# Optimization experiments

Measured on AMD Instinct MI355X. Metric: run time of the kernel, lower is better.

## Reference

```python
import jax, jax.numpy as jnp
from jax import lax
import numpy as np

N_NODES = 512
BATCH = 256
N_STEPS = 200
DT = 0.02  # t_span spacing; keeps 200 RK4 steps numerically tame


def setup_inputs() -> dict:
    key = jax.random.key(0)
    ks = jax.random.split(key, 7)
    s = 1.0 / np.sqrt(N_NODES)
    x_init = jax.random.normal(ks[0], (BATCH, N_NODES), dtype=jnp.float32)
    t_span = jnp.arange(N_STEPS, dtype=jnp.float32) * DT
    # MaskedLinear params (kaiming-uniform-ish scale)
    W1 = jax.random.uniform(ks[1], (N_NODES, N_NODES), jnp.float32, -s, s)
    b1 = jax.random.uniform(ks[2], (N_NODES,), jnp.float32, -s, s)
    # inner Linear params
    W2 = jax.random.uniform(ks[3], (N_NODES, N_NODES), jnp.float32, -s, s)
    b2 = jax.random.uniform(ks[4], (N_NODES,), jnp.float32, -s, s)
    mask = jax.random.bernoulli(ks[5], 0.1, (N_NODES, N_NODES)).astype(jnp.float32)
    mask = mask * (1.0 - jnp.eye(N_NODES, dtype=jnp.float32))
    return {"x_init": x_init, "t_span": t_span, "W1": W1, "b1": b1,
            "W2": W2, "b2": b2, "mask": mask}


def reference(x_init, t_span, W1, b1, W2, b2, mask):
    # ODE func: dydt = W2 @ tanh(masked(W1) @ y + b1) + b2 (t unused)
    Wm = W1 * mask  # [N, N]
    def f(y):  # y: [B, N]
        return jnp.tanh(y @ Wm.T + b1) @ W2.T + b2

    dts = t_span[1:] - t_span[:-1]  # [T-1]

    def rk4_step(y, dt):
        k1 = f(y)
        k2 = f(y + dt * k1 / 2)
        k3 = f(y + dt * k2 / 2)
        k4 = f(y + dt * k3)
        y_new = y + dt / 6 * (k1 + 2 * k2 + 2 * k3 + k4)
        return y_new, y_new

    _, traj = lax.scan(rk4_step, x_init, dts)  # [T-1, B, N]
    traj = jnp.concatenate([x_init[None], traj], axis=0)  # [T, B, N]
    return jnp.transpose(traj, (1, 0, 2))  # [B, T, N]
```

## Files before the change

### kernel.cpp

```cpp
#include <hip/hip_runtime.h>
#include <math.h>

#define NN 512
#define NB 256
#define NT 200
#define TPB 256
#define NTEAM 8

typedef unsigned long long u64;
typedef _Float16 half8 __attribute__((ext_vector_type(8)));
typedef float f32x4 __attribute__((ext_vector_type(4)));

#define WS_WM  0
#define WS_WC  (NN*NN)
#define WS_C   (WS_WC + NN*NN/2)
#define WS_X0  (WS_C + NN)
#define WS_HB0 (WS_X0 + NB*NN)
#define WS_CNT (WS_HB0 + NB*NN/2)

__device__ __forceinline__ void sysst_u64(u64* p, u64 v) {
  __hip_atomic_store(p, v, __ATOMIC_RELAXED, __HIP_MEMORY_SCOPE_SYSTEM);
}
__device__ __forceinline__ u64 sysld_u64(const u64* p) {
  return __hip_atomic_load(p, __ATOMIC_RELAXED, __HIP_MEMORY_SCOPE_SYSTEM);
}
__device__ __forceinline__ void sysst_f1(float* p, float v) {
  __hip_atomic_store(p, v, __ATOMIC_RELAXED, __HIP_MEMORY_SCOPE_SYSTEM);
}
__device__ __forceinline__ float sysld_f1(const float* p) {
  return __hip_atomic_load(p, __ATOMIC_RELAXED, __HIP_MEMORY_SCOPE_SYSTEM);
}
__device__ __forceinline__ void sysst_u16(unsigned short* p, unsigned short v) {
  __hip_atomic_store(p, v, __ATOMIC_RELAXED, __HIP_MEMORY_SCOPE_SYSTEM);
}
__device__ __forceinline__ void sysst_h(_Float16* p, float v) {
  union { _Float16 hf; unsigned short us; } cv; cv.hf = (_Float16)v;
  sysst_u16((unsigned short*)p, cv.us);
}

__global__ __launch_bounds__(256)
void k_init(const float* __restrict__ W1, const float* __restrict__ mask,
            const float* __restrict__ x_init, float* __restrict__ ws,
            float* __restrict__ out) {
  int gt = blockIdx.x * 256 + threadIdx.x;
  int stride = gridDim.x * 256;
  for (int i = gt; i < NN * NN; i += stride) ws[WS_WM + i] = W1[i] * mask[i];
  for (int i = gt; i < NB * NN / 2; i += stride) {
    u64 q = ((const u64*)x_init)[i];
    int r = i >> 8, np = i & 255;
    *((u64*)(out + (size_t)r * NT * NN) + np) = q;
  }
  if (gt < 64 * NTEAM * 16)
    __hip_atomic_store(((unsigned*)(ws + WS_CNT)) + gt, 0u,
                       __ATOMIC_RELAXED, __HIP_MEMORY_SCOPE_SYSTEM);
}

__global__ __launch_bounds__(128)
void k_prep(const float* __restrict__ W2g, const float* __restrict__ b2,
            const float* __restrict__ x_init, float* __restrict__ ws) {
  __shared__ float w1row[NN];
  const int j = blockIdx.x;
  const int t = threadIdx.x;
  const float* wm = ws + WS_WM + (size_t)j * NN;
  for (int i = t; i < NN; i += 128) w1row[i] = wm[i];
  __syncthreads();

  f32x4 acc = {0.f, 0.f, 0.f, 0.f};
  for (int m = 0; m < NN; ++m) {
    float w = w1row[m];
    if (w != 0.f)
      acc += w * ((const f32x4*)(W2g + (size_t)m * NN))[t];
  }
  _Float16* wcrow = (_Float16*)(ws + WS_WC) + (size_t)j * NN;
#pragma unroll
  for (int e = 0; e < 4; ++e) wcrow[4 * t + e] = (_Float16)acc[e];

  if (t == 0) {
    float s = 0.f;
    for (int m = 0; m < NN; ++m)
      if (w1row[m] != 0.f) s += b2[m] * w1row[m];
    ws[WS_C + j] = s;
  }

#pragma unroll
  for (int rr = 0; rr < 2; ++rr) {
    int r = t + rr * 128;
    const float* y0 = x_init + (size_t)r * NN;
    float s = 0.f;
    for (int m = 0; m < NN; ++m) {
      float w = w1row[m];
      if (w != 0.f) s = fmaf(y0[m], w, s);
    }
    sysst_f1(ws + WS_X0 + (size_t)r * NN + j, s);
  }
}

__device__ __forceinline__ void team_wait(unsigned* flagsp, unsigned target) {
  if (threadIdx.x < NTEAM) {
    while (__hip_atomic_load(flagsp + threadIdx.x * 16, __ATOMIC_RELAXED,
                             __HIP_MEMORY_SCOPE_AGENT) < target)
      __builtin_amdgcn_s_sleep(1);
  }
  __syncthreads();
}
__device__ __forceinline__ void team_release(unsigned* flagsp, int cg, unsigned e) {
  __syncthreads();
  if (threadIdx.x == 0)
    __hip_atomic_store(flagsp + cg * 16, e, __ATOMIC_RELAXED,
                       __HIP_MEMORY_SCOPE_SYSTEM);
}

struct St { u64 a0, a1; };
__device__ __forceinline__ St stage_load(const _Float16* __restrict__ src,
                                         int tid) {
  const int row = tid >> 6;
  const int g = tid & 63;
  const u64* s = (const u64*)(src + (size_t)row * NN) + g * 2;
  St v; v.a0 = sysld_u64(s); v.a1 = sysld_u64(s + 1);
  return v;
}
__device__ __forceinline__ void stage_write(_Float16* __restrict__ plane,
                                            const St& v, int tid) {
  const int row = tid >> 6;
  const int g = tid & 63;
  union { u64 q[2]; half8 h; } u; u.q[0] = v.a0; u.q[1] = v.a1;
  ((half8*)plane)[row * 64 + (g ^ row)] = u.h;
}

__device__ __forceinline__ void gemm8(const _Float16* plane, const _Float16* wb,
                                      int rc, int kg, int wv, float res[4]) {
  const int swzA = rc & 3;
  const int swzB = rc & 7;
  const half8* pA = (const half8*)plane;
  const half8* pB = (const half8*)wb;
  const int abase = (rc & 3) * 64;
  const int bbase = (wv * 16 + rc) * 64;
  f32x4 ae = {0.f, 0.f, 0.f, 0.f};
  f32x4 ao = {0.f, 0.f, 0.f, 0.f};
#pragma unroll
  for (int kt = 0; kt < 16; kt += 2) {
    const int k0 = kt * 4 + kg;
    const int k1 = (kt + 1) * 4 + kg;
    ae = __builtin_amdgcn_mfma_f32_16x16x32_f16(pA[abase + (k0 ^ swzA)],
                                                pB[bbase + (k0 ^ swzB)],
                                                ae, 0, 0, 0);
    ao = __builtin_amdgcn_mfma_f32_16x16x32_f16(pA[abase + (k1 ^ swzA)],
                                                pB[bbase + (k1 ^ swzB)],
                                                ao, 0, 0, 0);
  }
#pragma unroll
  for (int r = 0; r < 4; ++r) res[r] = ae[r] + ao[r];
}

__global__ __launch_bounds__(TPB, 1)
void k_ode(const float* __restrict__ tspan,
           const float* __restrict__ W2g,
           const float* __restrict__ b1,
           const float* __restrict__ b2,
           float* __restrict__ ws,
           float* __restrict__ out,
           const float* __restrict__ x_init) {
  extern __shared__ _Float16 ldsh[];
  _Float16* wc  = ldsh;
  _Float16* w2  = ldsh + 32768;
  _Float16* plA = ldsh + 65536;
  _Float16* plB = ldsh + 67584;

  const int bid = blockIdx.x;
  const int cg = bid & 7, rgA = bid >> 3;
  const int r0p[2] = {rgA * 4, rgA * 4 + 128};
  const int j0 = cg * 64;
  const int tid = threadIdx.x;
  const int lane = tid & 63, wv = tid >> 6;
  const int rc = lane & 15, kg = lane >> 4;
  const int mycol = j0 + wv * 16 + rc;
  const bool act = (kg == 0);

  unsigned* flbase = (unsigned*)(ws + WS_CNT);
  unsigned* flp[2] = {flbase + rgA * (NTEAM * 16),
                      flbase + (rgA + 32) * (NTEAM * 16)};
  _Float16* hb[2] = {(_Float16*)(ws + WS_HB0), (_Float16*)(ws + WS_WM)};

  {
    const int col = tid >> 2;
    const int part = tid & 3;
    const half8* s1 = (const half8*)((const _Float16*)(ws + WS_WC)
                                     + (size_t)(j0 + col) * NN) + part * 16;
    const float* s2 = W2g + (size_t)(j0 + col) * NN + part * 128;
    half8* d1 = (half8*)wc;
    half8* d2 = (half8*)w2;
    const int key = col & 7;
#pragma unroll
    for (int i = 0; i < 16; ++i) {
      int g = part * 16 + i;
      int idx = col * 64 + (g ^ key);
      d1[idx] = s1[i];
      half8 hv;
#pragma unroll
      for (int e = 0; e < 8; ++e) hv[e] = (_Float16)s2[i * 8 + e];
      d2[idx] = hv;
    }
  }
  const float b1s = b1[mycol], b2s = b2[mycol];
  const float c_own = ws[WS_C + mycol];

  float xb[2][4], yb[2][4], H[2][4];
  if (act) {
#pragma unroll
    for (int p = 0; p < 2; ++p)
#pragma unroll
      for (int r = 0; r < 4; ++r) {
        int row = r0p[p] + r;
        xb[p][r] = sysld_f1(ws + WS_X0 + (size_t)row * NN + mycol);
        yb[p][r] = x_init[(size_t)row * NN + mycol];
        float h = tanhf(xb[p][r] + b1s);
        H[p][r] = h;
        sysst_h(hb[0] + (size_t)row * NN + mycol, h);
      }
  }
  __syncthreads();
  if (tid == 0) {
    __hip_atomic_store(flp[0] + cg * 16, 1u, __ATOMIC_RELAXED,
                       __HIP_MEMORY_SCOPE_SYSTEM);
    __hip_atomic_store(flp[1] + cg * 16, 1u, __ATOMIC_RELAXED,
                       __HIP_MEMORY_SCOPE_SYSTEM);
  }

  float res[4], res2[4];

  for (int t = 0; t < NT - 1; ++t) {
    const float dt = tspan[t + 1] - tspan[t];
    const float c6 = dt / 6.0f;
#pragma unroll 1
    for (int s = 0; s < 4; ++s) {
      const int q = t * 4 + s;
      const unsigned target = (unsigned)(q + 1);
      const _Float16* rdb = hb[q & 1];
      _Float16* wrb = hb[(q + 1) & 1];

      team_wait(flp[0], target);
      St va = stage_load(rdb + (size_t)r0p[0] * NN, tid);
      team_wait(flp[1], target);
      St vb = stage_load(rdb + (size_t)r0p[1] * NN, tid);

      stage_write(plA, va, tid);
      __syncthreads();
      gemm8(plA, wc, rc, kg, wv, res);
      if (s == 3) gemm8(plA, w2, rc, kg, wv, res2);
      if (act) {
        if (s < 3) {
          const float a = (s == 2) ? dt : dt * 0.5f;
#pragma unroll
          for (int r = 0; r < 4; ++r) {
            float xs = xb[0][r] + a * (res[r] + c_own);
            float h = tanhf(xs + b1s);
            float st;
            if (s == 2) { H[0][r] += h;       st = H[0][r]; }
            else        { H[0][r] += 2.f * h; st = h;       }
            sysst_h(wrb + (size_t)(r0p[0] + r) * NN + mycol, st);
          }
        } else {
#pragma unroll
          for (int r = 0; r < 4; ++r) {
            int row = r0p[0] + r;
            xb[0][r] += c6 * res[r] + dt * c_own;
            yb[0][r] += c6 * res2[r] + dt * b2s;
            out[((size_t)row * NT + (t + 1)) * NN + mycol] = yb[0][r];
            float h = tanhf(xb[0][r] + b1s);
            H[0][r] = h;
            sysst_h(wrb + (size_t)row * NN + mycol, h);
          }
        }
      }
      team_release(flp[0], cg, target + 1);

      stage_write(plB, vb, tid);
      __syncthreads();
      gemm8(plB, wc, rc, kg, wv, res);
      if (s == 3) gemm8(plB, w2, rc, kg, wv, res2);
      if (act) {
        if (s < 3) {
          const float a = (s == 2) ? dt : dt * 0.5f;
#pragma unroll
          for (int r = 0; r < 4; ++r) {
            float xs = xb[1][r] + a * (res[r] + c_own);
            float h = tanhf(xs + b1s);
            float st;
            if (s == 2) { H[1][r] += h;       st = H[1][r]; }
            else        { H[1][r] += 2.f * h; st = h;       }
            sysst_h(wrb + (size_t)(r0p[1] + r) * NN + mycol, st);
          }
        } else {
#pragma unroll
          for (int r = 0; r < 4; ++r) {
            int row = r0p[1] + r;
            xb[1][r] += c6 * res[r] + dt * c_own;
            yb[1][r] += c6 * res2[r] + dt * b2s;
            out[((size_t)row * NT + (t + 1)) * NN + mycol] = yb[1][r];
            float h = tanhf(xb[1][r] + b1s);
            H[1][r] = h;
            sysst_h(wrb + (size_t)row * NN + mycol, h);
          }
        }
      }
      team_release(flp[1], cg, target + 1);
    }
  }
}

extern "C" void kernel_launch(void* const* d_in, const int* in_sizes, int n_in,
                              void* d_out, int out_size, void* d_ws, size_t ws_size,
                              hipStream_t stream) {
  const float* x_init = (const float*)d_in[0];
  const float* tspan  = (const float*)d_in[1];
  const float* W1     = (const float*)d_in[2];
  const float* b1     = (const float*)d_in[3];
  const float* W2     = (const float*)d_in[4];
  const float* b2     = (const float*)d_in[5];
  const float* mask   = (const float*)d_in[6];
  float* out = (float*)d_out;
  float* ws  = (float*)d_ws;

  hipLaunchKernelGGL(k_init, dim3(256), dim3(256), 0, stream,
                     W1, mask, x_init, ws, out);
  hipLaunchKernelGGL(k_prep, dim3(512), dim3(128), 0, stream,
                     W2, b2, x_init, ws);

  const unsigned ldsBytes = 136 * 1024;
  (void)hipFuncSetAttribute((const void*)k_ode,
                            hipFuncAttributeMaxDynamicSharedMemorySize,
                            (int)ldsBytes);

  hipLaunchKernelGGL(k_ode, dim3(256), dim3(TPB), ldsBytes, stream,
                     tspan, W2, b1, b2, ws, out, x_init);
}
```

Measured before the change: 2.668 ms.

## Replace team flag barriers with tagged data words for inter-block sync

Removes the per-team counter flags and the release/wait barriers. Each hidden-state exchange word now carries its step number in the upper 32 bits, next to two packed fp16 values, so consumers poll the data itself until every tag matches. The LDS staging planes are double-buffered by step parity so the release barrier can be dropped. This cuts flag round-trips and syncthreads per stage, at the cost of doubling exchange-buffer traffic (64-bit words for 2 halves) and extra shuffles to pack values.

```diff
diff --git a/kernel.cpp b/kernel.cpp
--- a/kernel.cpp
+++ b/kernel.cpp
@@ -5,7 +5,6 @@
 #define NB 256
 #define NT 200
 #define TPB 256
-#define NTEAM 8
 
 typedef unsigned long long u64;
 typedef _Float16 half8 __attribute__((ext_vector_type(8)));
@@ -16,7 +15,6 @@
 #define WS_C   (WS_WC + NN*NN/2)
 #define WS_X0  (WS_C + NN)
 #define WS_HB0 (WS_X0 + NB*NN)
-#define WS_CNT (WS_HB0 + NB*NN/2)
 
 __device__ __forceinline__ void sysst_u64(u64* p, u64 v) {
   __hip_atomic_store(p, v, __ATOMIC_RELAXED, __HIP_MEMORY_SCOPE_SYSTEM);
@@ -30,12 +28,10 @@
 __device__ __forceinline__ float sysld_f1(const float* p) {
   return __hip_atomic_load(p, __ATOMIC_RELAXED, __HIP_MEMORY_SCOPE_SYSTEM);
 }
-__device__ __forceinline__ void sysst_u16(unsigned short* p, unsigned short v) {
-  __hip_atomic_store(p, v, __ATOMIC_RELAXED, __HIP_MEMORY_SCOPE_SYSTEM);
-}
-__device__ __forceinline__ void sysst_h(_Float16* p, float v) {
-  union { _Float16 hf; unsigned short us; } cv; cv.hf = (_Float16)v;
-  sysst_u16((unsigned short*)p, cv.us);
+__device__ __forceinline__ u64 packh(float a, float b, unsigned tag) {
+  union { _Float16 h[2]; unsigned u; } lo;
+  lo.h[0] = (_Float16)a; lo.h[1] = (_Float16)b;
+  return ((u64)tag << 32) | (u64)lo.u;
 }
 
 __global__ __launch_bounds__(256)
@@ -50,9 +46,6 @@
     int r = i >> 8, np = i & 255;
     *((u64*)(out + (size_t)r * NT * NN) + np) = q;
   }
-  if (gt < 64 * NTEAM * 16)
-    __hip_atomic_store(((unsigned*)(ws + WS_CNT)) + gt, 0u,
-                       __ATOMIC_RELAXED, __HIP_MEMORY_SCOPE_SYSTEM);
 }
 
 __global__ __launch_bounds__(128)
@@ -95,36 +88,14 @@
   }
 }
 
-__device__ __forceinline__ void team_wait(unsigned* flagsp, unsigned target) {
-  if (threadIdx.x < NTEAM) {
-    while (__hip_atomic_load(flagsp + threadIdx.x * 16, __ATOMIC_RELAXED,
-                             __HIP_MEMORY_SCOPE_AGENT) < target)
-      __builtin_amdgcn_s_sleep(1);
-  }
-  __syncthreads();
-}
-__device__ __forceinline__ void team_release(unsigned* flagsp, int cg, unsigned e) {
-  __syncthreads();
-  if (threadIdx.x == 0)
-    __hip_atomic_store(flagsp + cg * 16, e, __ATOMIC_RELAXED,
-                       __HIP_MEMORY_SCOPE_SYSTEM);
-}
-
-struct St { u64 a0, a1; };
-__device__ __forceinline__ St stage_load(const _Float16* __restrict__ src,
-                                         int tid) {
-  const int row = tid >> 6;
-  const int g = tid & 63;
-  const u64* s = (const u64*)(src + (size_t)row * NN) + g * 2;
-  St v; v.a0 = sysld_u64(s); v.a1 = sysld_u64(s + 1);
-  return v;
-}
-__device__ __forceinline__ void stage_write(_Float16* __restrict__ plane,
-                                            const St& v, int tid) {
-  const int row = tid >> 6;
-  const int g = tid & 63;
-  union { u64 q[2]; half8 h; } u; u.q[0] = v.a0; u.q[1] = v.a1;
-  ((half8*)plane)[row * 64 + (g ^ row)] = u.h;
+__device__ __forceinline__ void unpack_write(_Float16* __restrict__ plane,
+                                             u64 v0, u64 v1, u64 v2, u64 v3,
+                                             int tid) {
+  const int row = tid >> 6, g = tid & 63;
+  union { unsigned u[4]; half8 h; } x;
+  x.u[0] = (unsigned)v0; x.u[1] = (unsigned)v1;
+  x.u[2] = (unsigned)v2; x.u[3] = (unsigned)v3;
+  ((half8*)plane)[row * 64 + (g ^ row)] = x.h;
 }
 
 __device__ __forceinline__ void gemm8(const _Float16* plane, const _Float16* wb,
@@ -161,10 +132,8 @@
            float* __restrict__ out,
            const float* __restrict__ x_init) {
   extern __shared__ _Float16 ldsh[];
-  _Float16* wc  = ldsh;
-  _Float16* w2  = ldsh + 32768;
-  _Float16* plA = ldsh + 65536;
-  _Float16* plB = ldsh + 67584;
+  _Float16* wc = ldsh;
+  _Float16* w2 = ldsh + 32768;
 
   const int bid = blockIdx.x;
   const int cg = bid & 7, rgA = bid >> 3;
@@ -176,10 +145,8 @@
   const int mycol = j0 + wv * 16 + rc;
   const bool act = (kg == 0);
 
-  unsigned* flbase = (unsigned*)(ws + WS_CNT);
-  unsigned* flp[2] = {flbase + rgA * (NTEAM * 16),
-                      flbase + (rgA + 32) * (NTEAM * 16)};
-  _Float16* hb[2] = {(_Float16*)(ws + WS_HB0), (_Float16*)(ws + WS_WM)};
+  u64* hbt0 = (u64*)(ws + WS_HB0);
+  u64* hbt1 = (u64*)(ws + WS_WM);
 
   {
     const int col = tid >> 2;
@@ -215,18 +182,16 @@
         yb[p][r] = x_init[(size_t)row * NN + mycol];
         float h = tanhf(xb[p][r] + b1s);
         H[p][r] = h;
-        sysst_h(hb[0] + (size_t)row * NN + mycol, h);
+        float hn = __shfl_down(h, 1);
+        if ((rc & 1) == 0)
+          sysst_u64(hbt0 + (size_t)row * 256 + (mycol >> 1), packh(h, hn, 0u));
       }
   }
   __syncthreads();
-  if (tid == 0) {
-    __hip_atomic_store(flp[0] + cg * 16, 1u, __ATOMIC_RELAXED,
-                       __HIP_MEMORY_SCOPE_SYSTEM);
-    __hip_atomic_store(flp[1] + cg * 16, 1u, __ATOMIC_RELAXED,
-                       __HIP_MEMORY_SCOPE_SYSTEM);
-  }
 
   float res[4], res2[4];
+  const int row_g = tid >> 6;
+  const int gidx = (tid & 63) * 4;
 
   for (int t = 0; t < NT - 1; ++t) {
     const float dt = tspan[t + 1] - tspan[t];
@@ -234,16 +199,29 @@
 #pragma unroll 1
     for (int s = 0; s < 4; ++s) {
       const int q = t * 4 + s;
-      const unsigned target = (unsigned)(q + 1);
-      const _Float16* rdb = hb[q & 1];
-      _Float16* wrb = hb[(q + 1) & 1];
-
-      team_wait(flp[0], target);
-      St va = stage_load(rdb + (size_t)r0p[0] * NN, tid);
-      team_wait(flp[1], target);
-      St vb = stage_load(rdb + (size_t)r0p[1] * NN, tid);
-
-      stage_write(plA, va, tid);
+      const unsigned wtag = (unsigned)(q + 1);
+      u64* rb = (q & 1) ? hbt1 : hbt0;
+      u64* wr = (q & 1) ? hbt0 : hbt1;
+      const u64* rdA = rb + (size_t)(r0p[0] + row_g) * 256 + gidx;
+      const u64* rdB = rb + (size_t)(r0p[1] + row_g) * 256 + gidx;
+      _Float16* plA = ldsh + 65536 + (q & 1) * 2048;
+      _Float16* plB = ldsh + 65536 + 4096 + (q & 1) * 2048;
+
+      u64 a0, a1, a2, a3;
+      for (;;) {
+        a0 = sysld_u64(rdA);     a1 = sysld_u64(rdA + 1);
+        a2 = sysld_u64(rdA + 2); a3 = sysld_u64(rdA + 3);
+        bool ok = ((unsigned)(a0 >> 32) == (unsigned)q) &
+                  ((unsigned)(a1 >> 32) == (unsigned)q) &
+                  ((unsigned)(a2 >> 32) == (unsigned)q) &
+                  ((unsigned)(a3 >> 32) == (unsigned)q);
+        if (__all(ok)) break;
+        __builtin_amdgcn_s_sleep(1);
+      }
+      u64 b0 = sysld_u64(rdB),       b1v_ = sysld_u64(rdB + 1);
+      u64 b2v_ = sysld_u64(rdB + 2), b3 = sysld_u64(rdB + 3);
+
+      unpack_write(plA, a0, a1, a2, a3, tid);
       __syncthreads();
       gemm8(plA, wc, rc, kg, wv, res);
       if (s == 3) gemm8(plA, w2, rc, kg, wv, res2);
@@ -257,7 +235,10 @@
             float st;
             if (s == 2) { H[0][r] += h;       st = H[0][r]; }
             else        { H[0][r] += 2.f * h; st = h;       }
-            sysst_h(wrb + (size_t)(r0p[0] + r) * NN + mycol, st);
+            float sn = __shfl_down(st, 1);
+            if ((rc & 1) == 0)
+              sysst_u64(wr + (size_t)(r0p[0] + r) * 256 + (mycol >> 1),
+                        packh(st, sn, wtag));
           }
         } else {
 #pragma unroll
@@ -268,13 +249,25 @@
             out[((size_t)row * NT + (t + 1)) * NN + mycol] = yb[0][r];
             float h = tanhf(xb[0][r] + b1s);
             H[0][r] = h;
-            sysst_h(wrb + (size_t)row * NN + mycol, h);
+            float hn = __shfl_down(h, 1);
+            if ((rc & 1) == 0)
+              sysst_u64(wr + (size_t)row * 256 + (mycol >> 1),
+                        packh(h, hn, wtag));
           }
         }
       }
-      team_release(flp[0], cg, target + 1);
-
-      stage_write(plB, vb, tid);
+
+      for (;;) {
+        bool ok = ((unsigned)(b0 >> 32) == (unsigned)q) &
+                  ((unsigned)(b1v_ >> 32) == (unsigned)q) &
+                  ((unsigned)(b2v_ >> 32) == (unsigned)q) &
+                  ((unsigned)(b3 >> 32) == (unsigned)q);
+        if (__all(ok)) break;
+        __builtin_amdgcn_s_sleep(1);
+        b0 = sysld_u64(rdB);       b1v_ = sysld_u64(rdB + 1);
+        b2v_ = sysld_u64(rdB + 2); b3 = sysld_u64(rdB + 3);
+      }
+      unpack_write(plB, b0, b1v_, b2v_, b3, tid);
       __syncthreads();
       gemm8(plB, wc, rc, kg, wv, res);
       if (s == 3) gemm8(plB, w2, rc, kg, wv, res2);
@@ -288,7 +281,10 @@
             float st;
             if (s == 2) { H[1][r] += h;       st = H[1][r]; }
             else        { H[1][r] += 2.f * h; st = h;       }
-            sysst_h(wrb + (size_t)(r0p[1] + r) * NN + mycol, st);
+            float sn = __shfl_down(st, 1);
+            if ((rc & 1) == 0)
+              sysst_u64(wr + (size_t)(r0p[1] + r) * 256 + (mycol >> 1),
+                        packh(st, sn, wtag));
           }
         } else {
 #pragma unroll
@@ -299,11 +295,13 @@
             out[((size_t)row * NT + (t + 1)) * NN + mycol] = yb[1][r];
             float h = tanhf(xb[1][r] + b1s);
             H[1][r] = h;
-            sysst_h(wrb + (size_t)row * NN + mycol, h);
+            float hn = __shfl_down(h, 1);
+            if ((rc & 1) == 0)
+              sysst_u64(wr + (size_t)row * 256 + (mycol >> 1),
+                        packh(h, hn, wtag));
           }
         }
       }
-      team_release(flp[1], cg, target + 1);
     }
   }
 }
@@ -326,7 +324,7 @@
   hipLaunchKernelGGL(k_prep, dim3(512), dim3(128), 0, stream,
                      W2, b2, x_init, ws);
 
-  const unsigned ldsBytes = 136 * 1024;
+  const unsigned ldsBytes = 144 * 1024;
   (void)hipFuncSetAttribute((const void*)k_ode,
                             hipFuncAttributeMaxDynamicSharedMemorySize,
                             (int)ldsBytes);
```

Measured after the change: 2.988 ms. 12.0% more time.
